# Kernel optimization log

Hardware: AMD Instinct MI355X
Metric: run time of the kernel (lower is better)

## Reference

```python
import jax, jax.numpy as jnp
import numpy as np

K = 3          # neighborhood kernel per axis
NUM_HEADS = 8
EPS = 1e-5     # InstanceNorm3d default eps


def _win_idx(D):
    """NATTEN-style clamped window: each query attends exactly K neighbors per axis."""
    i = jnp.arange(D)
    start = jnp.clip(i - K // 2, 0, D - K)
    idx = start[:, None] + jnp.arange(K)[None, :]   # (D, K) absolute neighbor coords
    rel = idx - i[:, None] + (K - 1)                # (D, K) in [0, 2K-2], rpb index
    return idx, rel


def setup_inputs() -> dict:
    key = jax.random.key(0)
    ks = jax.random.split(key, 6)
    B, C, H, W, Z = 1, 128, 64, 64, 8
    return {
        "x": jax.random.normal(ks[0], (B, C, H, W, Z), dtype=jnp.float32),
        "w_qkv": jax.random.normal(ks[1], (C, 3 * C), dtype=jnp.float32) * 0.02,
        "b_qkv": jnp.zeros((3 * C,), dtype=jnp.float32),
        "rpb": jax.random.normal(ks[2], (NUM_HEADS, 2 * K - 1, 2 * K - 1, 2 * K - 1), dtype=jnp.float32) * 0.02,
        "w_proj": jax.random.normal(ks[3], (C, C), dtype=jnp.float32) * 0.02,
        "b_proj": jnp.zeros((C,), dtype=jnp.float32),
    }


def reference(x, w_qkv, b_qkv, rpb, w_proj, b_proj):
    B, C, H, W, Z = x.shape
    h, hd = NUM_HEADS, C // NUM_HEADS
    # --- InstanceNorm3d (affine=False): normalize over spatial dims per (B, C) ---
    mu = x.mean(axis=(2, 3, 4), keepdims=True)
    var = x.var(axis=(2, 3, 4), keepdims=True)
    xn = (x - mu) * jax.lax.rsqrt(var + EPS)
    # --- qkv projection in channels-last token layout ---
    xt = jnp.transpose(xn, (0, 2, 3, 4, 1))                 # (B,H,W,Z,C)
    qkv = xt @ w_qkv + b_qkv                                 # (B,H,W,Z,3C)
    qkv = qkv.reshape(B, H, W, Z, 3, h, hd)
    qkv = jnp.transpose(qkv, (4, 0, 5, 1, 2, 3, 6))          # (3,B,h,H,W,Z,hd)
    q, k, v = qkv[0], qkv[1], qkv[2]
    q = q * (hd ** -0.5)
    # --- gather 3x3x3 neighborhoods (clamped at borders) ---
    ih, rh = _win_idx(H)
    iw, rw = _win_idx(W)
    iz, rz = _win_idx(Z)

    def gather_win(t):
        t = jnp.take(t, ih, axis=2)                          # (B,h,H,K,W,Z,hd)
        t = jnp.take(t, iw, axis=4)                          # (B,h,H,K,W,K,Z,hd)
        t = jnp.take(t, iz, axis=6)                          # (B,h,H,K,W,K,Z,K,hd)
        t = jnp.transpose(t, (0, 1, 2, 4, 6, 3, 5, 7, 8))    # (B,h,H,W,Z,K,K,K,hd)
        return t.reshape(B, h, H, W, Z, K * K * K, hd)

    kw = gather_win(k)
    vw = gather_win(v)
    # --- relative position bias, gathered per (query, neighbor) ---
    b = rpb[:, rh]                                           # (h,H,K,5,5)
    b = jnp.take(b, rw, axis=3)                              # (h,H,K,W,K,5)
    b = jnp.take(b, rz, axis=5)                              # (h,H,K,W,K,Z,K)
    b = jnp.transpose(b, (0, 1, 3, 5, 2, 4, 6)).reshape(h, H, W, Z, K * K * K)
    # --- neighborhood attention ---
    logits = jnp.einsum('bhxyzd,bhxyznd->bhxyzn', q, kw) + b
    attn = jax.nn.softmax(logits, axis=-1)
    out = jnp.einsum('bhxyzn,bhxyznd->bhxyzd', attn, vw)     # (B,h,H,W,Z,hd)
    out = jnp.transpose(out, (0, 2, 3, 4, 1, 5)).reshape(B, H, W, Z, C)
    out = out @ w_proj + b_proj
    return jnp.transpose(out, (0, 4, 1, 2, 3))               # (B,C,H,W,Z)
```

## Files before the change

kernel.cpp:

```cpp
#include <hip/hip_runtime.h>

#define HWZ 32768
#define NH 8

typedef __bf16 bf16x8 __attribute__((ext_vector_type(8)));
typedef unsigned short u16x8 __attribute__((ext_vector_type(8)));
typedef unsigned short u16x4 __attribute__((ext_vector_type(4)));
typedef short s16x4 __attribute__((ext_vector_type(4)));
typedef float f32x4 __attribute__((ext_vector_type(4)));

#define QKV_F_OFF 1024
#define HEADSZ (HWZ * 16)
#define REGSZ  (NH * HEADSZ)
#define WT_F_OFF  (QKV_F_OFF + (3 * REGSZ) / 2)
#define WQT_F_OFF (WT_F_OFF + 8192)

__device__ __forceinline__ unsigned short f2bf(float f) {
    unsigned int u = __builtin_bit_cast(unsigned int, f);
    unsigned int r = u + 0x7FFFu + ((u >> 16) & 1u);
    return (unsigned short)(r >> 16);
}

__global__ __launch_bounds__(512) void prep_kernel(const float* __restrict__ x,
                                                   const float* __restrict__ w_qkv,
                                                   const float* __restrict__ w_proj,
                                                   float* __restrict__ ws) {
    const int tid = threadIdx.x;
    const int bid = blockIdx.x;
    if (tid < 128) {
        if (bid < 384) {
            unsigned short* wqt = (unsigned short*)(ws + WQT_F_OFF);
            wqt[bid * 128 + tid] = f2bf(w_qkv[(size_t)tid * 384 + bid]);
        } else {
            int j = bid - 384;
            unsigned short* wpt = (unsigned short*)(ws + WT_F_OFF);
            wpt[j * 128 + tid] = f2bf(w_proj[(size_t)tid * 128 + j]);
        }
    }
    int c = bid >> 2, qtr = bid & 3;
    const float4* xp = (const float4*)(x + (size_t)c * HWZ + qtr * 8192);
    float s = 0.f, ss = 0.f;
#pragma unroll
    for (int i = 0; i < 4; i++) {
        float4 v = xp[tid + i * 512];
        s  += v.x + v.y + v.z + v.w;
        ss += v.x*v.x + v.y*v.y + v.z*v.z + v.w*v.w;
    }
    for (int off = 32; off; off >>= 1) {
        s  += __shfl_down(s, off);
        ss += __shfl_down(ss, off);
    }
    __shared__ float red[16];
    int lane = tid & 63, wid = tid >> 6;
    if (lane == 0) { red[wid] = s; red[8 + wid] = ss; }
    __syncthreads();
    if (tid == 0) {
        float S = 0.f, SS = 0.f;
        for (int w = 0; w < 8; w++) { S += red[w]; SS += red[8 + w]; }
        ws[c * 4 + qtr] = S;
        ws[512 + c * 4 + qtr] = SS;
    }
}

__global__ __launch_bounds__(512, 4) void qkv_kernel(const float* __restrict__ x,
                                                     const float* __restrict__ b_qkv,
                                                     float* __restrict__ ws) {
    __shared__ unsigned short xs[64 * 128];
    const int tid = threadIdx.x;
    const int p0 = blockIdx.x * 64;

    {
        const int pgrp = tid & 15;
        const int c0   = (tid >> 4) * 4;
        float mus[4], rss[4];
#pragma unroll
        for (int ci = 0; ci < 4; ci++) {
            float4 sp = *(const float4*)(ws + (c0 + ci) * 4);
            float4 sq = *(const float4*)(ws + 512 + (c0 + ci) * 4);
            float S  = sp.x + sp.y + sp.z + sp.w;
            float SS = sq.x + sq.y + sq.z + sq.w;
            float mu = S * (1.0f / HWZ);
            float var = SS * (1.0f / HWZ) - mu * mu;
            mus[ci] = mu;
            rss[ci] = rsqrtf(var + 1e-5f);
        }
        unsigned short vals[4][4];
#pragma unroll
        for (int ci = 0; ci < 4; ci++) {
            float4 v = *(const float4*)(x + (size_t)(c0 + ci) * HWZ + p0 + pgrp * 4);
            vals[ci][0] = f2bf((v.x - mus[ci]) * rss[ci]);
            vals[ci][1] = f2bf((v.y - mus[ci]) * rss[ci]);
            vals[ci][2] = f2bf((v.z - mus[ci]) * rss[ci]);
            vals[ci][3] = f2bf((v.w - mus[ci]) * rss[ci]);
        }
        const int c8 = c0 >> 3, cl = c0 & 7;
#pragma unroll
        for (int pi = 0; pi < 4; pi++) {
            int p = pgrp * 4 + pi;
            u16x4 o = {vals[0][pi], vals[1][pi], vals[2][pi], vals[3][pi]};
            *(u16x4*)(xs + p * 128 + ((c8 ^ (p & 15)) << 3) + cl) = o;
        }
    }
    __syncthreads();

    const int wv   = tid >> 6;
    const int lane = tid & 63;
    const int col  = lane & 15;
    const int kgrp = lane >> 4;
    const int ptile = wv & 3;
    const int jq    = wv >> 2;
    const unsigned short* arow = xs + (ptile * 16 + col) * 128;
    const int arow15 = (ptile * 16 + col) & 15;

    u16x8 a[4];
#pragma unroll
    for (int ks = 0; ks < 4; ks++) {
        a[ks] = *(const u16x8*)(arow + (((ks * 4 + kgrp) ^ arow15) << 3));
    }
    __syncthreads();

    const unsigned short* wqt = (const unsigned short*)(ws + WQT_F_OFF);
    unsigned short* qkvb = (unsigned short*)(ws + QKV_F_OFF);
    unsigned short* vsc = xs + wv * 320;
    const int rp_ = lane & 15, rdseg = lane >> 4;

    for (int chunk = 0; chunk < 3; chunk++) {
        float scale = (chunk == 0) ? 0.25f : 1.0f;
#pragma unroll
        for (int jt = 0; jt < 4; jt++) {
            int jl = jq * 64 + jt * 16 + col;
            const unsigned short* brow = wqt + (size_t)(chunk * 128 + jl) * 128;
            f32x4 acc = {0.f, 0.f, 0.f, 0.f};
#pragma unroll
            for (int ks = 0; ks < 4; ks++) {
                u16x8 b = *(const u16x8*)(brow + ((ks * 4 + kgrp) << 3));
                acc = __builtin_amdgcn_mfma_f32_16x16x32_bf16(
                        __builtin_bit_cast(bf16x8, a[ks]),
                        __builtin_bit_cast(bf16x8, b), acc, 0, 0, 0);
            }
            int head = jq * 4 + jt;
            float bias = b_qkv[chunk * 128 + head * 16 + col];
            if (chunk == 2) {
                unsigned short* vt = qkvb + 2 * (size_t)REGSZ
                                   + ((size_t)(head * 16 + col)) * HWZ
                                   + p0 + ptile * 16 + kgrp * 4;
                u16x4 o;
#pragma unroll
                for (int i = 0; i < 4; i++) o[i] = f2bf(acc[i] + bias);
                *(u16x4*)vt = o;
            } else {
#pragma unroll
                for (int i = 0; i < 4; i++) {
                    vsc[(kgrp * 4 + i) * 20 + col] = f2bf((acc[i] + bias) * scale);
                }
                asm volatile("s_waitcnt lgkmcnt(0)" ::: "memory");
                u16x4 vv = *(const u16x4*)(vsc + rp_ * 20 + rdseg * 4);
                unsigned short* dst = qkvb + (size_t)chunk * REGSZ + (size_t)head * HEADSZ
                                    + (size_t)(p0 + ptile * 16 + rp_) * 16 + rdseg * 4;
                *(u16x4*)dst = vv;
            }
        }
    }
}

__global__ __launch_bounds__(512, 4) void attnproj_kernel(const float* __restrict__ rpb,
                                                          const float* __restrict__ b_proj,
                                                          float* __restrict__ ws,
                                                          float* __restrict__ out) {
    __shared__ unsigned short aol[32 * 128];
    __shared__ float rpb_s[8 * 128];
    const int tid = threadIdx.x;

    const int bid = blockIdx.x;
    const int blk = (bid & 7) * 128 + (bid >> 3);

    for (int i = tid; i < 1024; i += 512) {
        int hh = i >> 7, e = i & 127;
        rpb_s[i] = (e < 125) ? rpb[hh * 125 + e] : 0.f;
    }
    __syncthreads();

    const int p0 = blk * 32;
    const int h0 = p0 >> 9;
    const int w0 = (p0 >> 3) & 63;
    const int wv = tid >> 6, lane = tid & 63;
    const int head = wv;
    const int g = lane >> 4;
    const int qcol = lane & 15;
    const int lw = qcol >> 3, qz = qcol & 7;
    const int z = qz;

    const int sh = min(max(h0 - 1, 0), 61);
    const int dh = sh - h0 + 2;
    const int sz = min(max(z - 1, 0), 5);
    unsigned zmask = 0;
#pragma unroll
    for (int zp = 0; zp < 8; zp++) {
        if (zp >= sz && zp <= sz + 2) zmask |= 1u << zp;
    }

    const unsigned short* qkvb = (const unsigned short*)(ws + QKV_F_OFF);
    const unsigned short* qbase = qkvb + (size_t)head * HEADSZ;
    const unsigned short* kbase = qkvb + (size_t)REGSZ + (size_t)head * HEADSZ;
    const unsigned short* vtb  = qkvb + 2 * (size_t)REGSZ + (size_t)(head * 16) * HWZ;
    const float* bt = rpb_s + head * 128;

    const int iwlA = qcol >> 3, zpA = qcol & 7;
    const int iwlV = g >> 1,   zp0V = (g & 1) * 4;

#pragma unroll 1
    for (int t = 0; t < 2; t++) {
        const int pt = p0 + t * 16;
        const int w0t = w0 + t * 2;
        const int w = w0t + lw;
        const int sw = min(max(w - 1, 0), 61);
        unsigned wmask = 0;
#pragma unroll
        for (int iw = 0; iw < 4; iw++) {
            int W = w0t - 1 + iw;
            if (W >= sw && W <= sw + 2) wmask |= 1u << iw;
        }
        int Wc[4];
#pragma unroll
        for (int iw = 0; iw < 4; iw++) Wc[iw] = min(max(w0t - 1 + iw, 0), 63);

        s16x4 bq = *(const s16x4*)(qbase + (size_t)(pt + qcol) * 16 + g * 4);
        s16x4 ak[6], av[6];
#pragma unroll
        for (int mt = 0; mt < 6; mt++) {
            int iwA = (mt & 1) * 2 + iwlA;
            int pkK = (sh + (mt >> 1)) * 512 + Wc[iwA] * 8 + zpA;
            ak[mt] = *(const s16x4*)(kbase + (size_t)pkK * 16 + g * 4);
            int iwV = (mt & 1) * 2 + iwlV;
            int pkV = (sh + (mt >> 1)) * 512 + Wc[iwV] * 8 + zp0V;
            av[mt] = *(const s16x4*)(vtb + (size_t)qcol * HWZ + pkV);
        }

        f32x4 acc[6];
#pragma unroll
        for (int mt = 0; mt < 6; mt++) {
            f32x4 zero = {0.f, 0.f, 0.f, 0.f};
            acc[mt] = __builtin_amdgcn_mfma_f32_16x16x16bf16_1k(ak[mt], bq, zero, 0, 0, 0);
        }

        float ssum = 0.f;
#pragma unroll
        for (int mt = 0; mt < 6; mt++) {
            int ih = mt >> 1;
#pragma unroll
            for (int r = 0; r < 4; r++) {
                int krow = g * 4 + r;
                int iw = (mt & 1) * 2 + (krow >> 3);
                int zp = krow & 7;
                int ok = ((wmask >> iw) & 1) & ((zmask >> zp) & 1);
                int idx = (dh + ih) * 25 + (iw + 1 - lw) * 5 + (zp - z + 2);
                idx = ok ? idx : 62;
                float lg = ok ? (acc[mt][r] + bt[idx]) : -1e30f;
                float pexp = __expf(lg);
                acc[mt][r] = pexp;
                ssum += pexp;
            }
        }
        ssum += __shfl_xor(ssum, 16);
        ssum += __shfl_xor(ssum, 32);
        float inv = 1.f / ssum;

        s16x4 pb[6];
#pragma unroll
        for (int mt = 0; mt < 6; mt++)
#pragma unroll
            for (int r = 0; r < 4; r++)
                pb[mt][r] = (short)f2bf(acc[mt][r]);

        f32x4 o0 = {0.f, 0.f, 0.f, 0.f}, o1 = {0.f, 0.f, 0.f, 0.f};
        o0 = __builtin_amdgcn_mfma_f32_16x16x16bf16_1k(av[0], pb[0], o0, 0, 0, 0);
        o1 = __builtin_amdgcn_mfma_f32_16x16x16bf16_1k(av[1], pb[1], o1, 0, 0, 0);
        o0 = __builtin_amdgcn_mfma_f32_16x16x16bf16_1k(av[2], pb[2], o0, 0, 0, 0);
        o1 = __builtin_amdgcn_mfma_f32_16x16x16bf16_1k(av[3], pb[3], o1, 0, 0, 0);
        o0 = __builtin_amdgcn_mfma_f32_16x16x16bf16_1k(av[4], pb[4], o0, 0, 0, 0);
        o1 = __builtin_amdgcn_mfma_f32_16x16x16bf16_1k(av[5], pb[5], o1, 0, 0, 0);
        f32x4 oacc = o0 + o1;

#pragma unroll
        for (int r = 0; r < 4; r++) {
            int c = head * 16 + g * 4 + r;
            aol[(t * 16 + qcol) * 128 + (((c >> 3) ^ qcol) << 3) + (c & 7)] = f2bf(oacc[r] * inv);
        }
    }

    const unsigned short* wpt = (const unsigned short*)(ws + WT_F_OFF);
    const int j = wv * 16 + qcol;
    const unsigned short* bp = wpt + j * 128;
    u16x8 b0 = *(const u16x8*)(bp + ((0 * 4 + g) << 3));
    u16x8 b1 = *(const u16x8*)(bp + ((1 * 4 + g) << 3));
    u16x8 b2 = *(const u16x8*)(bp + ((2 * 4 + g) << 3));
    u16x8 b3 = *(const u16x8*)(bp + ((3 * 4 + g) << 3));
    float bias = b_proj[j];
    __syncthreads();

#pragma unroll
    for (int t = 0; t < 2; t++) {
        const unsigned short* ap = aol + (t * 16 + qcol) * 128;
        u16x8 a[4];
#pragma unroll
        for (int ks = 0; ks < 4; ks++) {
            a[ks] = *(const u16x8*)(ap + (((ks * 4 + g) ^ qcol) << 3));
        }
        f32x4 p0a = {0.f, 0.f, 0.f, 0.f}, p1a = {0.f, 0.f, 0.f, 0.f};
        p0a = __builtin_amdgcn_mfma_f32_16x16x32_bf16(__builtin_bit_cast(bf16x8, a[0]),
                __builtin_bit_cast(bf16x8, b0), p0a, 0, 0, 0);
        p1a = __builtin_amdgcn_mfma_f32_16x16x32_bf16(__builtin_bit_cast(bf16x8, a[1]),
                __builtin_bit_cast(bf16x8, b1), p1a, 0, 0, 0);
        p0a = __builtin_amdgcn_mfma_f32_16x16x32_bf16(__builtin_bit_cast(bf16x8, a[2]),
                __builtin_bit_cast(bf16x8, b2), p0a, 0, 0, 0);
        p1a = __builtin_amdgcn_mfma_f32_16x16x32_bf16(__builtin_bit_cast(bf16x8, a[3]),
                __builtin_bit_cast(bf16x8, b3), p1a, 0, 0, 0);
        f32x4 pacc = p0a + p1a;

        float4 o4;
        o4.x = pacc[0] + bias; o4.y = pacc[1] + bias;
        o4.z = pacc[2] + bias; o4.w = pacc[3] + bias;
        *(float4*)(out + (size_t)j * HWZ + p0 + t * 16 + g * 4) = o4;
    }
}

extern "C" void kernel_launch(void* const* d_in, const int* in_sizes, int n_in,
                              void* d_out, int out_size, void* d_ws, size_t ws_size,
                              hipStream_t stream) {
    const float* x      = (const float*)d_in[0];
    const float* w_qkv  = (const float*)d_in[1];
    const float* b_qkv  = (const float*)d_in[2];
    const float* rpb    = (const float*)d_in[3];
    const float* w_proj = (const float*)d_in[4];
    const float* b_proj = (const float*)d_in[5];
    float* out = (float*)d_out;
    float* ws  = (float*)d_ws;

    prep_kernel<<<512, 512, 0, stream>>>(x, w_qkv, w_proj, ws);
    qkv_kernel<<<512, 512, 0, stream>>>(x, b_qkv, ws);
    attnproj_kernel<<<1024, 512, 0, stream>>>(rpb, b_proj, ws, out);
}
```

Baseline: 61.50 us.

## Fuse three kernels into one persistent kernel with grid barriers

Merges the stats/weight-prep, QKV projection and attention+projection kernels into a single 512-block kernel separated by atomic-counter grid barriers, with the attention stage looping over two tiles per block. The goal is to remove the launch gaps and tail effects between kernels. In exchange it adds a memset launch, global atomic spin-waits, and relies on all 512 blocks being co-resident (at 4 blocks per CU), otherwise it deadlocks.

After: 150.2 us. 144% more time.

```diff
diff --git a/kernel.cpp b/kernel.cpp
--- a/kernel.cpp
+++ b/kernel.cpp
@@ -9,7 +9,8 @@
 typedef short s16x4 __attribute__((ext_vector_type(4)));
 typedef float f32x4 __attribute__((ext_vector_type(4)));
 
-#define QKV_F_OFF 1024
+#define SYNC_F_OFF 1024
+#define QKV_F_OFF 2048
 #define HEADSZ (HWZ * 16)
 #define REGSZ  (NH * HEADSZ)
 #define WT_F_OFF  (QKV_F_OFF + (3 * REGSZ) / 2)
@@ -21,306 +22,324 @@
     return (unsigned short)(r >> 16);
 }
 
-__global__ __launch_bounds__(512) void prep_kernel(const float* __restrict__ x,
-                                                   const float* __restrict__ w_qkv,
-                                                   const float* __restrict__ w_proj,
-                                                   float* __restrict__ ws) {
+__device__ __forceinline__ void grid_barrier(int* cnt, int* flag, int nblocks) {
+    __syncthreads();
+    if (threadIdx.x == 0) {
+        __threadfence();
+        int old = atomicAdd(cnt, 1);
+        if (old == nblocks - 1) {
+            __hip_atomic_store(flag, 1, __ATOMIC_RELEASE, __HIP_MEMORY_SCOPE_AGENT);
+        } else {
+            while (__hip_atomic_load(flag, __ATOMIC_ACQUIRE, __HIP_MEMORY_SCOPE_AGENT) == 0) {
+                __builtin_amdgcn_s_sleep(2);
+            }
+        }
+        __threadfence();
+    }
+    __syncthreads();
+}
+
+__global__ __launch_bounds__(512, 4) void mega_kernel(
+        const float* __restrict__ x,      const float* __restrict__ w_qkv,
+        const float* __restrict__ b_qkv,  const float* __restrict__ rpb,
+        const float* __restrict__ w_proj, const float* __restrict__ b_proj,
+        float* __restrict__ ws,           float* __restrict__ out) {
+    __shared__ alignas(16) unsigned char smem[16384];
     const int tid = threadIdx.x;
     const int bid = blockIdx.x;
-    if (tid < 128) {
-        if (bid < 384) {
-            unsigned short* wqt = (unsigned short*)(ws + WQT_F_OFF);
-            wqt[bid * 128 + tid] = f2bf(w_qkv[(size_t)tid * 384 + bid]);
-        } else {
-            int j = bid - 384;
-            unsigned short* wpt = (unsigned short*)(ws + WT_F_OFF);
-            wpt[j * 128 + tid] = f2bf(w_proj[(size_t)tid * 128 + j]);
+    int* sync = (int*)(ws + SYNC_F_OFF);
+
+    {
+        if (tid < 128) {
+            if (bid < 384) {
+                unsigned short* wqt = (unsigned short*)(ws + WQT_F_OFF);
+                wqt[bid * 128 + tid] = f2bf(w_qkv[(size_t)tid * 384 + bid]);
+            } else {
+                int j = bid - 384;
+                unsigned short* wpt = (unsigned short*)(ws + WT_F_OFF);
+                wpt[j * 128 + tid] = f2bf(w_proj[(size_t)tid * 128 + j]);
+            }
+        }
+        int c = bid >> 2, qtr = bid & 3;
+        const float4* xp = (const float4*)(x + (size_t)c * HWZ + qtr * 8192);
+        float s = 0.f, ss = 0.f;
+#pragma unroll
+        for (int i = 0; i < 4; i++) {
+            float4 v = xp[tid + i * 512];
+            s  += v.x + v.y + v.z + v.w;
+            ss += v.x*v.x + v.y*v.y + v.z*v.z + v.w*v.w;
+        }
+        for (int off = 32; off; off >>= 1) {
+            s  += __shfl_down(s, off);
+            ss += __shfl_down(ss, off);
+        }
+        float* red = (float*)smem;
+        int lane = tid & 63, wid = tid >> 6;
+        if (lane == 0) { red[wid] = s; red[8 + wid] = ss; }
+        __syncthreads();
+        if (tid == 0) {
+            float S = 0.f, SS = 0.f;
+            for (int w = 0; w < 8; w++) { S += red[w]; SS += red[8 + w]; }
+            ws[c * 4 + qtr] = S;
+            ws[512 + c * 4 + qtr] = SS;
         }
     }
-    int c = bid >> 2, qtr = bid & 3;
-    const float4* xp = (const float4*)(x + (size_t)c * HWZ + qtr * 8192);
-    float s = 0.f, ss = 0.f;
-#pragma unroll
-    for (int i = 0; i < 4; i++) {
-        float4 v = xp[tid + i * 512];
-        s  += v.x + v.y + v.z + v.w;
-        ss += v.x*v.x + v.y*v.y + v.z*v.z + v.w*v.w;
+    grid_barrier(&sync[0], &sync[1], 512);
+
+    {
+        unsigned short* xs = (unsigned short*)smem;
+        const int p0 = bid * 64;
+        {
+            const int pgrp = tid & 15;
+            const int c0   = (tid >> 4) * 4;
+            float mus[4], rss[4];
+#pragma unroll
+            for (int ci = 0; ci < 4; ci++) {
+                float4 sp = *(const float4*)(ws + (c0 + ci) * 4);
+                float4 sq = *(const float4*)(ws + 512 + (c0 + ci) * 4);
+                float S  = sp.x + sp.y + sp.z + sp.w;
+                float SS = sq.x + sq.y + sq.z + sq.w;
+                float mu = S * (1.0f / HWZ);
+                float var = SS * (1.0f / HWZ) - mu * mu;
+                mus[ci] = mu;
+                rss[ci] = rsqrtf(var + 1e-5f);
+            }
+            unsigned short vals[4][4];
+#pragma unroll
+            for (int ci = 0; ci < 4; ci++) {
+                float4 v = *(const float4*)(x + (size_t)(c0 + ci) * HWZ + p0 + pgrp * 4);
+                vals[ci][0] = f2bf((v.x - mus[ci]) * rss[ci]);
+                vals[ci][1] = f2bf((v.y - mus[ci]) * rss[ci]);
+                vals[ci][2] = f2bf((v.z - mus[ci]) * rss[ci]);
+                vals[ci][3] = f2bf((v.w - mus[ci]) * rss[ci]);
+            }
+            const int c8 = c0 >> 3, cl = c0 & 7;
+#pragma unroll
+            for (int pi = 0; pi < 4; pi++) {
+                int p = pgrp * 4 + pi;
+                u16x4 o = {vals[0][pi], vals[1][pi], vals[2][pi], vals[3][pi]};
+                *(u16x4*)(xs + p * 128 + ((c8 ^ (p & 15)) << 3) + cl) = o;
+            }
+        }
+        __syncthreads();
+
+        const int wv   = tid >> 6;
+        const int lane = tid & 63;
+        const int col  = lane & 15;
+        const int kgrp = lane >> 4;
+        const int ptile = wv & 3;
+        const int jq    = wv >> 2;
+        const unsigned short* arow = xs + (ptile * 16 + col) * 128;
+        const int arow15 = (ptile * 16 + col) & 15;
+
+        u16x8 a[4];
+#pragma unroll
+        for (int ks = 0; ks < 4; ks++) {
+            a[ks] = *(const u16x8*)(arow + (((ks * 4 + kgrp) ^ arow15) << 3));
+        }
+        __syncthreads();
+
+        const unsigned short* wqt = (const unsigned short*)(ws + WQT_F_OFF);
+        unsigned short* qkvb = (unsigned short*)(ws + QKV_F_OFF);
+        unsigned short* vsc = xs + wv * 320;
+        const int rp_ = lane & 15, rdseg = lane >> 4;
+
+        for (int chunk = 0; chunk < 3; chunk++) {
+            float scale = (chunk == 0) ? 0.25f : 1.0f;
+#pragma unroll
+            for (int jt = 0; jt < 4; jt++) {
+                int jl = jq * 64 + jt * 16 + col;
+                const unsigned short* brow = wqt + (size_t)(chunk * 128 + jl) * 128;
+                f32x4 acc = {0.f, 0.f, 0.f, 0.f};
+#pragma unroll
+                for (int ks = 0; ks < 4; ks++) {
+                    u16x8 b = *(const u16x8*)(brow + ((ks * 4 + kgrp) << 3));
+                    acc = __builtin_amdgcn_mfma_f32_16x16x32_bf16(
+                            __builtin_bit_cast(bf16x8, a[ks]),
+                            __builtin_bit_cast(bf16x8, b), acc, 0, 0, 0);
+                }
+                int head = jq * 4 + jt;
+                float bias = b_qkv[chunk * 128 + head * 16 + col];
+                if (chunk == 2) {
+                    unsigned short* vt = qkvb + 2 * (size_t)REGSZ
+                                       + ((size_t)(head * 16 + col)) * HWZ
+                                       + p0 + ptile * 16 + kgrp * 4;
+                    u16x4 o;
+#pragma unroll
+                    for (int i = 0; i < 4; i++) o[i] = f2bf(acc[i] + bias);
+                    *(u16x4*)vt = o;
+                } else {
+#pragma unroll
+                    for (int i = 0; i < 4; i++) {
+                        vsc[(kgrp * 4 + i) * 20 + col] = f2bf((acc[i] + bias) * scale);
+                    }
+                    asm volatile("s_waitcnt lgkmcnt(0)" ::: "memory");
+                    u16x4 vv = *(const u16x4*)(vsc + rp_ * 20 + rdseg * 4);
+                    unsigned short* dst = qkvb + (size_t)chunk * REGSZ + (size_t)head * HEADSZ
+                                        + (size_t)(p0 + ptile * 16 + rp_) * 16 + rdseg * 4;
+                    *(u16x4*)dst = vv;
+                }
+            }
+        }
     }
-    for (int off = 32; off; off >>= 1) {
-        s  += __shfl_down(s, off);
-        ss += __shfl_down(ss, off);
-    }
-    __shared__ float red[16];
-    int lane = tid & 63, wid = tid >> 6;
-    if (lane == 0) { red[wid] = s; red[8 + wid] = ss; }
-    __syncthreads();
-    if (tid == 0) {
-        float S = 0.f, SS = 0.f;
-        for (int w = 0; w < 8; w++) { S += red[w]; SS += red[8 + w]; }
-        ws[c * 4 + qtr] = S;
-        ws[512 + c * 4 + qtr] = SS;
-    }
-}
-
-__global__ __launch_bounds__(512, 4) void qkv_kernel(const float* __restrict__ x,
-                                                     const float* __restrict__ b_qkv,
-                                                     float* __restrict__ ws) {
-    __shared__ unsigned short xs[64 * 128];
-    const int tid = threadIdx.x;
-    const int p0 = blockIdx.x * 64;
+    grid_barrier(&sync[2], &sync[3], 512);
 
     {
-        const int pgrp = tid & 15;
-        const int c0   = (tid >> 4) * 4;
-        float mus[4], rss[4];
-#pragma unroll
-        for (int ci = 0; ci < 4; ci++) {
-            float4 sp = *(const float4*)(ws + (c0 + ci) * 4);
-            float4 sq = *(const float4*)(ws + 512 + (c0 + ci) * 4);
-            float S  = sp.x + sp.y + sp.z + sp.w;
-            float SS = sq.x + sq.y + sq.z + sq.w;
-            float mu = S * (1.0f / HWZ);
-            float var = SS * (1.0f / HWZ) - mu * mu;
-            mus[ci] = mu;
-            rss[ci] = rsqrtf(var + 1e-5f);
-        }
-        unsigned short vals[4][4];
-#pragma unroll
-        for (int ci = 0; ci < 4; ci++) {
-            float4 v = *(const float4*)(x + (size_t)(c0 + ci) * HWZ + p0 + pgrp * 4);
-            vals[ci][0] = f2bf((v.x - mus[ci]) * rss[ci]);
-            vals[ci][1] = f2bf((v.y - mus[ci]) * rss[ci]);
-            vals[ci][2] = f2bf((v.z - mus[ci]) * rss[ci]);
-            vals[ci][3] = f2bf((v.w - mus[ci]) * rss[ci]);
-        }
-        const int c8 = c0 >> 3, cl = c0 & 7;
-#pragma unroll
-        for (int pi = 0; pi < 4; pi++) {
-            int p = pgrp * 4 + pi;
-            u16x4 o = {vals[0][pi], vals[1][pi], vals[2][pi], vals[3][pi]};
-            *(u16x4*)(xs + p * 128 + ((c8 ^ (p & 15)) << 3) + cl) = o;
-        }
-    }
-    __syncthreads();
-
-    const int wv   = tid >> 6;
-    const int lane = tid & 63;
-    const int col  = lane & 15;
-    const int kgrp = lane >> 4;
-    const int ptile = wv & 3;
-    const int jq    = wv >> 2;
-    const unsigned short* arow = xs + (ptile * 16 + col) * 128;
-    const int arow15 = (ptile * 16 + col) & 15;
-
-    u16x8 a[4];
-#pragma unroll
-    for (int ks = 0; ks < 4; ks++) {
-        a[ks] = *(const u16x8*)(arow + (((ks * 4 + kgrp) ^ arow15) << 3));
-    }
-    __syncthreads();
-
-    const unsigned short* wqt = (const unsigned short*)(ws + WQT_F_OFF);
-    unsigned short* qkvb = (unsigned short*)(ws + QKV_F_OFF);
-    unsigned short* vsc = xs + wv * 320;
-    const int rp_ = lane & 15, rdseg = lane >> 4;
-
-    for (int chunk = 0; chunk < 3; chunk++) {
-        float scale = (chunk == 0) ? 0.25f : 1.0f;
-#pragma unroll
-        for (int jt = 0; jt < 4; jt++) {
-            int jl = jq * 64 + jt * 16 + col;
-            const unsigned short* brow = wqt + (size_t)(chunk * 128 + jl) * 128;
-            f32x4 acc = {0.f, 0.f, 0.f, 0.f};
-#pragma unroll
-            for (int ks = 0; ks < 4; ks++) {
-                u16x8 b = *(const u16x8*)(brow + ((ks * 4 + kgrp) << 3));
-                acc = __builtin_amdgcn_mfma_f32_16x16x32_bf16(
-                        __builtin_bit_cast(bf16x8, a[ks]),
-                        __builtin_bit_cast(bf16x8, b), acc, 0, 0, 0);
-            }
-            int head = jq * 4 + jt;
-            float bias = b_qkv[chunk * 128 + head * 16 + col];
-            if (chunk == 2) {
-                unsigned short* vt = qkvb + 2 * (size_t)REGSZ
-                                   + ((size_t)(head * 16 + col)) * HWZ
-                                   + p0 + ptile * 16 + kgrp * 4;
-                u16x4 o;
-#pragma unroll
-                for (int i = 0; i < 4; i++) o[i] = f2bf(acc[i] + bias);
-                *(u16x4*)vt = o;
-            } else {
-#pragma unroll
-                for (int i = 0; i < 4; i++) {
-                    vsc[(kgrp * 4 + i) * 20 + col] = f2bf((acc[i] + bias) * scale);
-                }
-                asm volatile("s_waitcnt lgkmcnt(0)" ::: "memory");
-                u16x4 vv = *(const u16x4*)(vsc + rp_ * 20 + rdseg * 4);
-                unsigned short* dst = qkvb + (size_t)chunk * REGSZ + (size_t)head * HEADSZ
-                                    + (size_t)(p0 + ptile * 16 + rp_) * 16 + rdseg * 4;
-                *(u16x4*)dst = vv;
-            }
-        }
-    }
-}
-
-__global__ __launch_bounds__(512, 4) void attnproj_kernel(const float* __restrict__ rpb,
-                                                          const float* __restrict__ b_proj,
-                                                          float* __restrict__ ws,
-                                                          float* __restrict__ out) {
-    __shared__ unsigned short aol[32 * 128];
-    __shared__ float rpb_s[8 * 128];
-    const int tid = threadIdx.x;
-
-    const int bid = blockIdx.x;
-    const int blk = (bid & 7) * 128 + (bid >> 3);
-
-    for (int i = tid; i < 1024; i += 512) {
-        int hh = i >> 7, e = i & 127;
-        rpb_s[i] = (e < 125) ? rpb[hh * 125 + e] : 0.f;
-    }
-    __syncthreads();
-
-    const int p0 = blk * 32;
-    const int h0 = p0 >> 9;
-    const int w0 = (p0 >> 3) & 63;
-    const int wv = tid >> 6, lane = tid & 63;
-    const int head = wv;
-    const int g = lane >> 4;
-    const int qcol = lane & 15;
-    const int lw = qcol >> 3, qz = qcol & 7;
-    const int z = qz;
-
-    const int sh = min(max(h0 - 1, 0), 61);
-    const int dh = sh - h0 + 2;
-    const int sz = min(max(z - 1, 0), 5);
-    unsigned zmask = 0;
-#pragma unroll
-    for (int zp = 0; zp < 8; zp++) {
-        if (zp >= sz && zp <= sz + 2) zmask |= 1u << zp;
-    }
-
-    const unsigned short* qkvb = (const unsigned short*)(ws + QKV_F_OFF);
-    const unsigned short* qbase = qkvb + (size_t)head * HEADSZ;
-    const unsigned short* kbase = qkvb + (size_t)REGSZ + (size_t)head * HEADSZ;
-    const unsigned short* vtb  = qkvb + 2 * (size_t)REGSZ + (size_t)(head * 16) * HWZ;
-    const float* bt = rpb_s + head * 128;
-
-    const int iwlA = qcol >> 3, zpA = qcol & 7;
-    const int iwlV = g >> 1,   zp0V = (g & 1) * 4;
+        unsigned short* aol = (unsigned short*)smem;
+        float* rpb_s = (float*)(smem + 8192);
+        for (int i = tid; i < 1024; i += 512) {
+            int hh = i >> 7, e = i & 127;
+            rpb_s[i] = (e < 125) ? rpb[hh * 125 + e] : 0.f;
+        }
+        __syncthreads();
+
+        const int wv = tid >> 6, lane = tid & 63;
+        const int head = wv;
+        const int g = lane >> 4;
+        const int qcol = lane & 15;
+        const int lw = qcol >> 3, qz = qcol & 7;
+        const int z = qz;
+        const int sz = min(max(z - 1, 0), 5);
+        unsigned zmask = 0;
+#pragma unroll
+        for (int zp = 0; zp < 8; zp++) {
+            if (zp >= sz && zp <= sz + 2) zmask |= 1u << zp;
+        }
+
+        const unsigned short* qkvb = (const unsigned short*)(ws + QKV_F_OFF);
+        const unsigned short* qbase = qkvb + (size_t)head * HEADSZ;
+        const unsigned short* kbase = qkvb + (size_t)REGSZ + (size_t)head * HEADSZ;
+        const unsigned short* vtb  = qkvb + 2 * (size_t)REGSZ + (size_t)(head * 16) * HWZ;
+        const float* bt = rpb_s + head * 128;
+        const unsigned short* wpt = (const unsigned short*)(ws + WT_F_OFF);
+        const int j = wv * 16 + qcol;
+
+        const int iwlA = qcol >> 3, zpA = qcol & 7;
+        const int iwlV = g >> 1,   zp0V = (g & 1) * 4;
 
 #pragma unroll 1
-    for (int t = 0; t < 2; t++) {
-        const int pt = p0 + t * 16;
-        const int w0t = w0 + t * 2;
-        const int w = w0t + lw;
-        const int sw = min(max(w - 1, 0), 61);
-        unsigned wmask = 0;
-#pragma unroll
-        for (int iw = 0; iw < 4; iw++) {
-            int W = w0t - 1 + iw;
-            if (W >= sw && W <= sw + 2) wmask |= 1u << iw;
-        }
-        int Wc[4];
-#pragma unroll
-        for (int iw = 0; iw < 4; iw++) Wc[iw] = min(max(w0t - 1 + iw, 0), 63);
-
-        s16x4 bq = *(const s16x4*)(qbase + (size_t)(pt + qcol) * 16 + g * 4);
-        s16x4 ak[6], av[6];
-#pragma unroll
-        for (int mt = 0; mt < 6; mt++) {
-            int iwA = (mt & 1) * 2 + iwlA;
-            int pkK = (sh + (mt >> 1)) * 512 + Wc[iwA] * 8 + zpA;
-            ak[mt] = *(const s16x4*)(kbase + (size_t)pkK * 16 + g * 4);
-            int iwV = (mt & 1) * 2 + iwlV;
-            int pkV = (sh + (mt >> 1)) * 512 + Wc[iwV] * 8 + zp0V;
-            av[mt] = *(const s16x4*)(vtb + (size_t)qcol * HWZ + pkV);
-        }
-
-        f32x4 acc[6];
-#pragma unroll
-        for (int mt = 0; mt < 6; mt++) {
-            f32x4 zero = {0.f, 0.f, 0.f, 0.f};
-            acc[mt] = __builtin_amdgcn_mfma_f32_16x16x16bf16_1k(ak[mt], bq, zero, 0, 0, 0);
-        }
-
-        float ssum = 0.f;
-#pragma unroll
-        for (int mt = 0; mt < 6; mt++) {
-            int ih = mt >> 1;
-#pragma unroll
-            for (int r = 0; r < 4; r++) {
-                int krow = g * 4 + r;
-                int iw = (mt & 1) * 2 + (krow >> 3);
-                int zp = krow & 7;
-                int ok = ((wmask >> iw) & 1) & ((zmask >> zp) & 1);
-                int idx = (dh + ih) * 25 + (iw + 1 - lw) * 5 + (zp - z + 2);
-                idx = ok ? idx : 62;
-                float lg = ok ? (acc[mt][r] + bt[idx]) : -1e30f;
-                float pexp = __expf(lg);
-                acc[mt][r] = pexp;
-                ssum += pexp;
-            }
-        }
-        ssum += __shfl_xor(ssum, 16);
-        ssum += __shfl_xor(ssum, 32);
-        float inv = 1.f / ssum;
-
-        s16x4 pb[6];
-#pragma unroll
-        for (int mt = 0; mt < 6; mt++)
-#pragma unroll
-            for (int r = 0; r < 4; r++)
-                pb[mt][r] = (short)f2bf(acc[mt][r]);
-
-        f32x4 o0 = {0.f, 0.f, 0.f, 0.f}, o1 = {0.f, 0.f, 0.f, 0.f};
-        o0 = __builtin_amdgcn_mfma_f32_16x16x16bf16_1k(av[0], pb[0], o0, 0, 0, 0);
-        o1 = __builtin_amdgcn_mfma_f32_16x16x16bf16_1k(av[1], pb[1], o1, 0, 0, 0);
-        o0 = __builtin_amdgcn_mfma_f32_16x16x16bf16_1k(av[2], pb[2], o0, 0, 0, 0);
-        o1 = __builtin_amdgcn_mfma_f32_16x16x16bf16_1k(av[3], pb[3], o1, 0, 0, 0);
-        o0 = __builtin_amdgcn_mfma_f32_16x16x16bf16_1k(av[4], pb[4], o0, 0, 0, 0);
-        o1 = __builtin_amdgcn_mfma_f32_16x16x16bf16_1k(av[5], pb[5], o1, 0, 0, 0);
-        f32x4 oacc = o0 + o1;
-
-#pragma unroll
-        for (int r = 0; r < 4; r++) {
-            int c = head * 16 + g * 4 + r;
-            aol[(t * 16 + qcol) * 128 + (((c >> 3) ^ qcol) << 3) + (c & 7)] = f2bf(oacc[r] * inv);
-        }
-    }
-
-    const unsigned short* wpt = (const unsigned short*)(ws + WT_F_OFF);
-    const int j = wv * 16 + qcol;
-    const unsigned short* bp = wpt + j * 128;
-    u16x8 b0 = *(const u16x8*)(bp + ((0 * 4 + g) << 3));
-    u16x8 b1 = *(const u16x8*)(bp + ((1 * 4 + g) << 3));
-    u16x8 b2 = *(const u16x8*)(bp + ((2 * 4 + g) << 3));
-    u16x8 b3 = *(const u16x8*)(bp + ((3 * 4 + g) << 3));
-    float bias = b_proj[j];
-    __syncthreads();
-
-#pragma unroll
-    for (int t = 0; t < 2; t++) {
-        const unsigned short* ap = aol + (t * 16 + qcol) * 128;
-        u16x8 a[4];
-#pragma unroll
-        for (int ks = 0; ks < 4; ks++) {
-            a[ks] = *(const u16x8*)(ap + (((ks * 4 + g) ^ qcol) << 3));
-        }
-        f32x4 p0a = {0.f, 0.f, 0.f, 0.f}, p1a = {0.f, 0.f, 0.f, 0.f};
-        p0a = __builtin_amdgcn_mfma_f32_16x16x32_bf16(__builtin_bit_cast(bf16x8, a[0]),
-                __builtin_bit_cast(bf16x8, b0), p0a, 0, 0, 0);
-        p1a = __builtin_amdgcn_mfma_f32_16x16x32_bf16(__builtin_bit_cast(bf16x8, a[1]),
-                __builtin_bit_cast(bf16x8, b1), p1a, 0, 0, 0);
-        p0a = __builtin_amdgcn_mfma_f32_16x16x32_bf16(__builtin_bit_cast(bf16x8, a[2]),
-                __builtin_bit_cast(bf16x8, b2), p0a, 0, 0, 0);
-        p1a = __builtin_amdgcn_mfma_f32_16x16x32_bf16(__builtin_bit_cast(bf16x8, a[3]),
-                __builtin_bit_cast(bf16x8, b3), p1a, 0, 0, 0);
-        f32x4 pacc = p0a + p1a;
-
-        float4 o4;
-        o4.x = pacc[0] + bias; o4.y = pacc[1] + bias;
-        o4.z = pacc[2] + bias; o4.w = pacc[3] + bias;
-        *(float4*)(out + (size_t)j * HWZ + p0 + t * 16 + g * 4) = o4;
+        for (int it = 0; it < 2; it++) {
+            const int blk = (bid & 7) * 128 + (bid >> 3) * 2 + it;
+            const int p0 = blk * 32;
+            const int h0 = p0 >> 9;
+            const int w0 = (p0 >> 3) & 63;
+            const int sh = min(max(h0 - 1, 0), 61);
+            const int dh = sh - h0 + 2;
+
+#pragma unroll 1
+            for (int t = 0; t < 2; t++) {
+                const int pt = p0 + t * 16;
+                const int w0t = w0 + t * 2;
+                const int w = w0t + lw;
+                const int sw = min(max(w - 1, 0), 61);
+                unsigned wmask = 0;
+#pragma unroll
+                for (int iw = 0; iw < 4; iw++) {
+                    int W = w0t - 1 + iw;
+                    if (W >= sw && W <= sw + 2) wmask |= 1u << iw;
+                }
+                int Wc[4];
+#pragma unroll
+                for (int iw = 0; iw < 4; iw++) Wc[iw] = min(max(w0t - 1 + iw, 0), 63);
+
+                s16x4 bq = *(const s16x4*)(qbase + (size_t)(pt + qcol) * 16 + g * 4);
+                s16x4 ak[6], av[6];
+#pragma unroll
+                for (int mt = 0; mt < 6; mt++) {
+                    int iwA = (mt & 1) * 2 + iwlA;
+                    int pkK = (sh + (mt >> 1)) * 512 + Wc[iwA] * 8 + zpA;
+                    ak[mt] = *(const s16x4*)(kbase + (size_t)pkK * 16 + g * 4);
+                    int iwV = (mt & 1) * 2 + iwlV;
+                    int pkV = (sh + (mt >> 1)) * 512 + Wc[iwV] * 8 + zp0V;
+                    av[mt] = *(const s16x4*)(vtb + (size_t)qcol * HWZ + pkV);
+                }
+
+                f32x4 acc[6];
+#pragma unroll
+                for (int mt = 0; mt < 6; mt++) {
+                    f32x4 zero = {0.f, 0.f, 0.f, 0.f};
+                    acc[mt] = __builtin_amdgcn_mfma_f32_16x16x16bf16_1k(ak[mt], bq, zero, 0, 0, 0);
+                }
+
+                float ssum = 0.f;
+#pragma unroll
+                for (int mt = 0; mt < 6; mt++) {
+                    int ih = mt >> 1;
+#pragma unroll
+                    for (int r = 0; r < 4; r++) {
+                        int krow = g * 4 + r;
+                        int iw = (mt & 1) * 2 + (krow >> 3);
+                        int zp = krow & 7;
+                        int ok = ((wmask >> iw) & 1) & ((zmask >> zp) & 1);
+                        int idx = (dh + ih) * 25 + (iw + 1 - lw) * 5 + (zp - z + 2);
+                        idx = ok ? idx : 62;
+                        float lg = ok ? (acc[mt][r] + bt[idx]) : -1e30f;
+                        float pexp = __expf(lg);
+                        acc[mt][r] = pexp;
+                        ssum += pexp;
+                    }
+                }
+                ssum += __shfl_xor(ssum, 16);
+                ssum += __shfl_xor(ssum, 32);
+                float inv = 1.f / ssum;
+
+                s16x4 pb[6];
+#pragma unroll
+                for (int mt = 0; mt < 6; mt++)
+#pragma unroll
+                    for (int r = 0; r < 4; r++)
+                        pb[mt][r] = (short)f2bf(acc[mt][r]);
+
+                f32x4 o0 = {0.f, 0.f, 0.f, 0.f}, o1 = {0.f, 0.f, 0.f, 0.f};
+                o0 = __builtin_amdgcn_mfma_f32_16x16x16bf16_1k(av[0], pb[0], o0, 0, 0, 0);
+                o1 = __builtin_amdgcn_mfma_f32_16x16x16bf16_1k(av[1], pb[1], o1, 0, 0, 0);
+                o0 = __builtin_amdgcn_mfma_f32_16x16x16bf16_1k(av[2], pb[2], o0, 0, 0, 0);
+                o1 = __builtin_amdgcn_mfma_f32_16x16x16bf16_1k(av[3], pb[3], o1, 0, 0, 0);
+                o0 = __builtin_amdgcn_mfma_f32_16x16x16bf16_1k(av[4], pb[4], o0, 0, 0, 0);
+                o1 = __builtin_amdgcn_mfma_f32_16x16x16bf16_1k(av[5], pb[5], o1, 0, 0, 0);
+                f32x4 oacc = o0 + o1;
+
+#pragma unroll
+                for (int r = 0; r < 4; r++) {
+                    int c = head * 16 + g * 4 + r;
+                    aol[(t * 16 + qcol) * 128 + (((c >> 3) ^ qcol) << 3) + (c & 7)] = f2bf(oacc[r] * inv);
+                }
+            }
+
+            const unsigned short* bp = wpt + j * 128;
+            u16x8 b0 = *(const u16x8*)(bp + ((0 * 4 + g) << 3));
+            u16x8 b1 = *(const u16x8*)(bp + ((1 * 4 + g) << 3));
+            u16x8 b2 = *(const u16x8*)(bp + ((2 * 4 + g) << 3));
+            u16x8 b3 = *(const u16x8*)(bp + ((3 * 4 + g) << 3));
+            float bias = b_proj[j];
+            __syncthreads();
+
+#pragma unroll
+            for (int t = 0; t < 2; t++) {
+                const unsigned short* ap = aol + (t * 16 + qcol) * 128;
+                u16x8 a[4];
+#pragma unroll
+                for (int ks = 0; ks < 4; ks++) {
+                    a[ks] = *(const u16x8*)(ap + (((ks * 4 + g) ^ qcol) << 3));
+                }
+                f32x4 p0a = {0.f, 0.f, 0.f, 0.f}, p1a = {0.f, 0.f, 0.f, 0.f};
+                p0a = __builtin_amdgcn_mfma_f32_16x16x32_bf16(__builtin_bit_cast(bf16x8, a[0]),
+                        __builtin_bit_cast(bf16x8, b0), p0a, 0, 0, 0);
+                p1a = __builtin_amdgcn_mfma_f32_16x16x32_bf16(__builtin_bit_cast(bf16x8, a[1]),
+                        __builtin_bit_cast(bf16x8, b1), p1a, 0, 0, 0);
+                p0a = __builtin_amdgcn_mfma_f32_16x16x32_bf16(__builtin_bit_cast(bf16x8, a[2]),
+                        __builtin_bit_cast(bf16x8, b2), p0a, 0, 0, 0);
+                p1a = __builtin_amdgcn_mfma_f32_16x16x32_bf16(__builtin_bit_cast(bf16x8, a[3]),
+                        __builtin_bit_cast(bf16x8, b3), p1a, 0, 0, 0);
+                f32x4 pacc = p0a + p1a;
+
+                float4 o4;
+                o4.x = pacc[0] + bias; o4.y = pacc[1] + bias;
+                o4.z = pacc[2] + bias; o4.w = pacc[3] + bias;
+                *(float4*)(out + (size_t)j * HWZ + p0 + t * 16 + g * 4) = o4;
+            }
+            __syncthreads();
+        }
     }
 }
 
@@ -336,7 +355,6 @@
     float* out = (float*)d_out;
     float* ws  = (float*)d_ws;
 
-    prep_kernel<<<512, 512, 0, stream>>>(x, w_qkv, w_proj, ws);
-    qkv_kernel<<<512, 512, 0, stream>>>(x, b_qkv, ws);
-    attnproj_kernel<<<1024, 512, 0, stream>>>(rpb, b_proj, ws, out);
+    hipMemsetAsync((void*)(ws + SYNC_F_OFF), 0, 16, stream);
+    mega_kernel<<<512, 512, 0, stream>>>(x, w_qkv, b_qkv, rpb, w_proj, b_proj, ws, out);
 }
```
